# Kernel tuning notes

Hardware: AMD Instinct MI355X
Metric: run time of the kernel (lower is better)

## Reference

```python
import jax, jax.numpy as jnp
import numpy as np

NEG_SLOPE = 0.2


def gat_conv(x, src, dst, W, att_src, att_dst, bias, heads, out_ch, concat, N):
    # Linear transform: [N, heads, out_ch]
    h = (x @ W).reshape(N, heads, out_ch)
    # Per-node attention logits [N, heads]
    a_s = jnp.einsum('nhc,hc->nh', h, att_src)
    a_d = jnp.einsum('nhc,hc->nh', h, att_dst)
    # Per-edge logits: edge j->i uses src j, dst i
    e = jax.nn.leaky_relu(a_s[src] + a_d[dst], NEG_SLOPE)  # [E, heads]
    # Segment softmax over destination neighborhoods
    m = jax.ops.segment_max(e, dst, num_segments=N)  # [N, heads]
    ex = jnp.exp(e - m[dst])
    denom = jax.ops.segment_sum(ex, dst, num_segments=N)
    alpha = ex / denom[dst]  # [E, heads]
    # Weighted message scatter-add
    out = jax.ops.segment_sum(h[src] * alpha[:, :, None], dst, num_segments=N)  # [N, heads, out_ch]
    out = out.reshape(N, heads * out_ch) if concat else out.mean(axis=1)
    return out + bias


def setup_inputs() -> dict:
    key = jax.random.key(0)
    ks = jax.random.split(key, 12)
    N, E, F_IN, HID, HEADS, NCLS = 100000, 1600000, 256, 16, 8, 32
    x = jax.random.normal(ks[0], (N, F_IN), dtype=jnp.float32)
    edge_index = jax.random.randint(ks[1], (2, E), 0, N, dtype=jnp.int32)
    edge_weight = jax.random.uniform(ks[2], (E,), dtype=jnp.float32)
    s1 = 1.0 / np.sqrt(F_IN)
    W1 = jax.random.normal(ks[3], (F_IN, HEADS * HID), dtype=jnp.float32) * s1
    att_src1 = jax.random.normal(ks[4], (HEADS, HID), dtype=jnp.float32) * 0.1
    att_dst1 = jax.random.normal(ks[5], (HEADS, HID), dtype=jnp.float32) * 0.1
    b1 = jnp.zeros((HEADS * HID,), dtype=jnp.float32)
    s2 = 1.0 / np.sqrt(HEADS * HID)
    W2 = jax.random.normal(ks[6], (HEADS * HID, NCLS), dtype=jnp.float32) * s2
    att_src2 = jax.random.normal(ks[7], (1, NCLS), dtype=jnp.float32) * 0.1
    att_dst2 = jax.random.normal(ks[8], (1, NCLS), dtype=jnp.float32) * 0.1
    b2 = jnp.zeros((NCLS,), dtype=jnp.float32)
    return {"x": x, "edge_index": edge_index, "edge_weight": edge_weight,
            "W1": W1, "att_src1": att_src1, "att_dst1": att_dst1, "b1": b1,
            "W2": W2, "att_src2": att_src2, "att_dst2": att_dst2, "b2": b2}


def reference(x, edge_index, edge_weight, W1, att_src1, att_dst1, b1, W2, att_src2, att_dst2, b2):
    N = x.shape[0]
    # PyG GATConv add_self_loops=True: append self-loops once (used by both layers)
    loop = jnp.arange(N, dtype=edge_index.dtype)
    src = jnp.concatenate([edge_index[0], loop])
    dst = jnp.concatenate([edge_index[1], loop])
    # eval mode: dropout is identity; edge_weight unused by GATConv
    h = gat_conv(x, src, dst, W1, att_src1, att_dst1, b1, heads=8, out_ch=16, concat=True, N=N)
    h = jax.nn.elu(h)
    out = gat_conv(h, src, dst, W2, att_src2, att_dst2, b2, heads=1, out_ch=32, concat=False, N=N)
    return jax.nn.log_softmax(out, axis=-1)
```

## Files before the change

kernel.cpp:

```cpp
#include <hip/hip_runtime.h>
#include <hip/hip_fp16.h>
#include <math.h>

#define NEG_SLOPE 0.2f
#define NBLK 256

typedef _Float16 half8 __attribute__((ext_vector_type(8)));
typedef _Float16 half4 __attribute__((ext_vector_type(4)));
typedef float f32x4 __attribute__((ext_vector_type(4)));
typedef float f32x2 __attribute__((ext_vector_type(2)));

__device__ __forceinline__ float lrelu(float x){ return x > 0.f ? x : NEG_SLOPE*x; }

__global__ void k_prepw(const float* __restrict__ W, _Float16* __restrict__ Wt){
  int t = blockIdx.x*blockDim.x + threadIdx.x;
  int c = t >> 8, k = t & 255;
  Wt[t] = (_Float16)W[k*128 + c];
}

__global__ __launch_bounds__(256) void k_gemm1(const float* __restrict__ x,
                                               const _Float16* __restrict__ Wt,
                                               _Float16* __restrict__ h1h, int N){
  __shared__ _Float16 aL[2][128*40];
  __shared__ _Float16 bL[2][128*40];
  int tid = threadIdx.x;
  int w = tid >> 6, lane = tid & 63;
  int fq = lane >> 4, fr = lane & 15;
  int row0 = blockIdx.x * 128;
  f32x4 acc[2][8];
  #pragma unroll
  for (int m=0;m<2;m++)
    #pragma unroll
    for (int n=0;n<8;n++) acc[m][n] = (f32x4){0.f,0.f,0.f,0.f};

  int rA = tid>>3, kcA = (tid&7)*4;
  float4 va[4]; half8 vb[2];

  #pragma unroll
  for (int it=0; it<4; it++){
    int gr = row0 + it*32 + rA;
    va[it] = make_float4(0.f,0.f,0.f,0.f);
    if (gr < N) va[it] = *(const float4*)&x[(size_t)gr*256 + kcA];
  }
  #pragma unroll
  for (int it=0; it<2; it++){
    int chunk = it*256 + tid;
    vb[it] = *(const half8*)&Wt[(size_t)(chunk>>2)*256 + (chunk&3)*8];
  }
  #pragma unroll
  for (int it=0; it<4; it++){
    half4 hv; hv[0]=(_Float16)va[it].x; hv[1]=(_Float16)va[it].y;
    hv[2]=(_Float16)va[it].z; hv[3]=(_Float16)va[it].w;
    *(half4*)&aL[0][(it*32+rA)*40 + kcA] = hv;
  }
  #pragma unroll
  for (int it=0; it<2; it++){
    int chunk = it*256 + tid;
    *(half8*)&bL[0][(chunk>>2)*40 + (chunk&3)*8] = vb[it];
  }
  __syncthreads();

  int cur = 0;
  for (int ki=0; ki<8; ki++){
    int kk = ki*32;
    if (ki < 7){
      #pragma unroll
      for (int it=0; it<4; it++){
        int gr = row0 + it*32 + rA;
        va[it] = make_float4(0.f,0.f,0.f,0.f);
        if (gr < N) va[it] = *(const float4*)&x[(size_t)gr*256 + kk + 32 + kcA];
      }
      #pragma unroll
      for (int it=0; it<2; it++){
        int chunk = it*256 + tid;
        vb[it] = *(const half8*)&Wt[(size_t)(chunk>>2)*256 + kk + 32 + (chunk&3)*8];
      }
    }
    int kb = fq*8;
    half8 afrag[2], bfrag[8];
    #pragma unroll
    for (int m=0;m<2;m++) afrag[m] = *(half8*)&aL[cur][(w*32 + m*16 + fr)*40 + kb];
    #pragma unroll
    for (int n=0;n<8;n++) bfrag[n] = *(half8*)&bL[cur][(n*16 + fr)*40 + kb];
    #pragma unroll
    for (int m=0;m<2;m++)
      #pragma unroll
      for (int n=0;n<8;n++)
        acc[m][n] = __builtin_amdgcn_mfma_f32_16x16x32_f16(afrag[m], bfrag[n], acc[m][n], 0, 0, 0);
    if (ki < 7){
      #pragma unroll
      for (int it=0; it<4; it++){
        half4 hv; hv[0]=(_Float16)va[it].x; hv[1]=(_Float16)va[it].y;
        hv[2]=(_Float16)va[it].z; hv[3]=(_Float16)va[it].w;
        *(half4*)&aL[cur^1][(it*32+rA)*40 + kcA] = hv;
      }
      #pragma unroll
      for (int it=0; it<2; it++){
        int chunk = it*256 + tid;
        *(half8*)&bL[cur^1][(chunk>>2)*40 + (chunk&3)*8] = vb[it];
      }
      __syncthreads();
      cur ^= 1;
    }
  }
  #pragma unroll
  for (int m=0;m<2;m++){
    #pragma unroll
    for (int j=0;j<4;j++){
      int gr = row0 + w*32 + m*16 + fq*4 + j;
      if (gr < N){
        #pragma unroll
        for (int n=0;n<8;n++)
          h1h[(size_t)gr*128 + n*16 + fr] = (_Float16)acc[m][n][j];
      }
    }
  }
}

__global__ void k_cvt8(const _Float16* __restrict__ h1h,
                       const float* __restrict__ as_w, const float* __restrict__ ad_w,
                       unsigned* __restrict__ h1p, float* __restrict__ a_s,
                       float* __restrict__ a_d, int N){
  int t = blockIdx.x*blockDim.x + threadIdx.x;
  if (t >= N*16) return;
  int row = t >> 4, c8 = t & 15;
  half8 hv = *(const half8*)&h1h[(size_t)row*128 + c8*8];
  float f[8];
  #pragma unroll
  for (int j=0;j<8;j++) f[j] = (float)hv[j];
  int w0 = 0, w1 = 0;
  w0 = __builtin_amdgcn_cvt_pk_fp8_f32(f[0], f[1], w0, false);
  w0 = __builtin_amdgcn_cvt_pk_fp8_f32(f[2], f[3], w0, true);
  w1 = __builtin_amdgcn_cvt_pk_fp8_f32(f[4], f[5], w1, false);
  w1 = __builtin_amdgcn_cvt_pk_fp8_f32(f[6], f[7], w1, true);
  *(uint2*)&h1p[(size_t)row*32 + c8*2] = make_uint2((unsigned)w0,(unsigned)w1);
  int head = c8 >> 1;
  const float* wsp = &as_w[head*16 + (c8&1)*8];
  const float* wdp = &ad_w[head*16 + (c8&1)*8];
  float s=0.f, d=0.f;
  #pragma unroll
  for (int j=0;j<8;j++){ s = fmaf(f[j], wsp[j], s); d = fmaf(f[j], wdp[j], d); }
  s += __shfl_xor(s, 1);
  d += __shfl_xor(d, 1);
  if ((c8&1)==0){ a_s[(size_t)row*8+head]=s; a_d[(size_t)row*8+head]=d; }
}

__global__ __launch_bounds__(256) void k_bh(const int* __restrict__ dst, int* __restrict__ bh,
                                            int E, int EE, int NB){
  __shared__ int h[1024];
  int tid = threadIdx.x, blk = blockIdx.x;
  for (int i=tid;i<1024;i+=256) h[i]=0;
  __syncthreads();
  int chunk = (EE + NBLK - 1)/NBLK;
  int e0 = blk*chunk, e1 = min(e0+chunk, EE);
  for (int e=e0+tid; e<e1; e+=256){
    int d = (e<E)? dst[e] : (e-E);
    atomicAdd(&h[d>>7], 1);
  }
  __syncthreads();
  for (int i=tid;i<NB;i+=256) bh[i*NBLK + blk] = h[i];
}

__global__ __launch_bounds__(256) void k_scanA(int* __restrict__ bh, int* __restrict__ btot){
  __shared__ int t[256];
  int b = blockIdx.x, tid = threadIdx.x;
  int v = bh[b*NBLK + tid];
  t[tid] = v;
  __syncthreads();
  for (int off=1; off<256; off<<=1){
    int p = (tid>=off)? t[tid-off] : 0;
    __syncthreads();
    t[tid] += p;
    __syncthreads();
  }
  bh[b*NBLK + tid] = t[tid] - v;
  if (tid==255) btot[b] = t[255];
}

__global__ __launch_bounds__(256) void k_bscan(const int* __restrict__ btot, int* __restrict__ bbase,
                                               int* __restrict__ start_, int NB, int N, int EE){
  __shared__ int t[256];
  int tid = threadIdx.x;
  int i0 = tid*4;
  int a0 = (i0+0<NB)? btot[i0+0] : 0;
  int a1 = (i0+1<NB)? btot[i0+1] : 0;
  int a2 = (i0+2<NB)? btot[i0+2] : 0;
  int a3 = (i0+3<NB)? btot[i0+3] : 0;
  int s = a0+a1+a2+a3;
  t[tid] = s;
  __syncthreads();
  for (int off=1; off<256; off<<=1){
    int p = (tid>=off)? t[tid-off] : 0;
    __syncthreads();
    t[tid] += p;
    __syncthreads();
  }
  int excl = t[tid] - s;
  int e0=excl, e1=e0+a0, e2=e1+a1, e3=e2+a2;
  if (i0+0<NB) bbase[i0+0]=e0;
  if (i0+1<NB) bbase[i0+1]=e1;
  if (i0+2<NB) bbase[i0+2]=e2;
  if (i0+3<NB) bbase[i0+3]=e3;
  if (tid==0){ bbase[NB] = EE; start_[N] = EE; }
}

__global__ __launch_bounds__(256) void k_bfill(const int* __restrict__ src, const int* __restrict__ dst,
                       const int* __restrict__ bh, const int* __restrict__ bbase,
                       unsigned* __restrict__ pairs, int E, int EE, int NB){
  __shared__ int cur[1024];
  int tid = threadIdx.x, blk = blockIdx.x;
  for (int i=tid;i<NB;i+=256) cur[i] = bbase[i] + bh[i*NBLK + blk];
  __syncthreads();
  int chunk = (EE + NBLK - 1)/NBLK;
  int e0 = blk*chunk, e1 = min(e0+chunk, EE);
  for (int e=e0+tid; e<e1; e+=256){
    int s,d;
    if (e<E){ s=src[e]; d=dst[e]; } else { s=e-E; d=s; }
    int p = atomicAdd(&cur[d>>7], 1);
    pairs[p] = ((unsigned)s << 7) | (unsigned)(d & 127);
  }
}

__global__ __launch_bounds__(256) void k_pb(const int* __restrict__ bbase, const unsigned* __restrict__ pairs,
                    int* __restrict__ start_, int* __restrict__ csr_src, int N){
  __shared__ int hist[128];
  __shared__ int excl[128];
  int b = blockIdx.x;
  int tid = threadIdx.x;
  int base = bbase[b], cnt = bbase[b+1] - base;
  if (tid<128) hist[tid]=0;
  __syncthreads();
  for (int i=tid;i<cnt;i+=256){
    unsigned p = pairs[base+i];
    atomicAdd(&hist[p & 127], 1);
  }
  __syncthreads();
  if (tid < 128) excl[tid] = hist[tid];
  __syncthreads();
  for (int off=1; off<128; off<<=1){
    int p=0;
    if (tid<128 && tid>=off) p = excl[tid-off];
    __syncthreads();
    if (tid<128) excl[tid] += p;
    __syncthreads();
  }
  if (tid < 128){
    int e = excl[tid] - hist[tid];
    int node = (b<<7) + tid;
    if (node < N) start_[node] = base + e;
    hist[tid] = e;
  }
  __syncthreads();
  for (int i=tid;i<cnt;i+=256){
    unsigned p = pairs[base+i];
    int pos = atomicAdd(&hist[p & 127], 1);
    csr_src[base + pos] = (int)(p >> 7);
  }
}

__global__ __launch_bounds__(256) void k_agg1(const int* __restrict__ start, const int* __restrict__ csr_src,
                      const float* __restrict__ a_s, const float* __restrict__ a_d,
                      const unsigned* __restrict__ h1p, _Float16* __restrict__ acc1h, int N){
  int wid = (blockIdx.x*blockDim.x + threadIdx.x) >> 6;
  int lane = threadIdx.x & 63;
  if (wid >= N) return;
  int d = wid;
  int half = lane >> 5;
  int l32  = lane & 31;
  int head = l32 >> 2;
  float ad = a_d[(size_t)d*8 + head];
  int beg = start[d], end = start[d+1];
  float ax=0.f, ay=0.f, az=0.f, aw=0.f, den=0.f;
  int j = beg + half;
  for (; j + 6 < end; j += 8){
    int s0 = csr_src[j];
    int s1 = csr_src[j+2];
    int s2 = csr_src[j+4];
    int s3 = csr_src[j+6];
    float e0 = __expf(lrelu(a_s[(size_t)s0*8 + head] + ad));
    float e1 = __expf(lrelu(a_s[(size_t)s1*8 + head] + ad));
    float e2 = __expf(lrelu(a_s[(size_t)s2*8 + head] + ad));
    float e3 = __expf(lrelu(a_s[(size_t)s3*8 + head] + ad));
    unsigned u0 = h1p[(size_t)s0*32 + l32];
    unsigned u1 = h1p[(size_t)s1*32 + l32];
    unsigned u2 = h1p[(size_t)s2*32 + l32];
    unsigned u3 = h1p[(size_t)s3*32 + l32];
    f32x2 l0 = __builtin_amdgcn_cvt_pk_f32_fp8((int)u0, false), h0 = __builtin_amdgcn_cvt_pk_f32_fp8((int)u0, true);
    f32x2 l1 = __builtin_amdgcn_cvt_pk_f32_fp8((int)u1, false), h1 = __builtin_amdgcn_cvt_pk_f32_fp8((int)u1, true);
    f32x2 l2 = __builtin_amdgcn_cvt_pk_f32_fp8((int)u2, false), h2 = __builtin_amdgcn_cvt_pk_f32_fp8((int)u2, true);
    f32x2 l3 = __builtin_amdgcn_cvt_pk_f32_fp8((int)u3, false), h3 = __builtin_amdgcn_cvt_pk_f32_fp8((int)u3, true);
    ax = fmaf(e0, l0.x, ax); ay = fmaf(e0, l0.y, ay); az = fmaf(e0, h0.x, az); aw = fmaf(e0, h0.y, aw);
    ax = fmaf(e1, l1.x, ax); ay = fmaf(e1, l1.y, ay); az = fmaf(e1, h1.x, az); aw = fmaf(e1, h1.y, aw);
    ax = fmaf(e2, l2.x, ax); ay = fmaf(e2, l2.y, ay); az = fmaf(e2, h2.x, az); aw = fmaf(e2, h2.y, aw);
    ax = fmaf(e3, l3.x, ax); ay = fmaf(e3, l3.y, ay); az = fmaf(e3, h3.x, az); aw = fmaf(e3, h3.y, aw);
    den += (e0 + e1) + (e2 + e3);
  }
  for (; j < end; j += 2){
    int s0 = csr_src[j];
    float e0 = __expf(lrelu(a_s[(size_t)s0*8 + head] + ad));
    unsigned u0 = h1p[(size_t)s0*32 + l32];
    f32x2 l0 = __builtin_amdgcn_cvt_pk_f32_fp8((int)u0, false), h0 = __builtin_amdgcn_cvt_pk_f32_fp8((int)u0, true);
    ax = fmaf(e0, l0.x, ax); ay = fmaf(e0, l0.y, ay); az = fmaf(e0, h0.x, az); aw = fmaf(e0, h0.y, aw);
    den += e0;
  }
  ax += __shfl_xor(ax, 32);
  ay += __shfl_xor(ay, 32);
  az += __shfl_xor(az, 32);
  aw += __shfl_xor(aw, 32);
  den += __shfl_xor(den, 32);
  float inv = (den > 0.f) ? 1.f/den : 0.f;
  if (half == 0){
    half4 o;
    o[0]=(_Float16)(ax*inv); o[1]=(_Float16)(ay*inv);
    o[2]=(_Float16)(az*inv); o[3]=(_Float16)(aw*inv);
    *(half4*)&acc1h[(size_t)d*128 + l32*4] = o;
  }
}

__global__ __launch_bounds__(256) void k_layer2(const _Float16* __restrict__ acc1h, const float* __restrict__ b1,
                        const float* __restrict__ W2, const float* __restrict__ as2w,
                        const float* __restrict__ ad2w,
                        __half* __restrict__ h2ph, float* __restrict__ a_s2,
                        float* __restrict__ a_d2, int N){
  __shared__ float w2s[128][32];
  __shared__ float hs[8][128];
  int tid = threadIdx.x;
  #pragma unroll
  for (int it=0; it<16; it++){
    int idx = it*256 + tid;
    ((float*)w2s)[idx] = W2[idx];
  }
  int sub = tid>>5, ln = tid&31;
  int n = blockIdx.x*8 + sub;
  if (n < N){
    half4 hv = *(const half4*)&acc1h[(size_t)n*128 + ln*4];
    float4 bb = *(const float4*)&b1[ln*4];
    float v0 = (float)hv[0] + bb.x;
    float v1 = (float)hv[1] + bb.y;
    float v2 = (float)hv[2] + bb.z;
    float v3 = (float)hv[3] + bb.w;
    hs[sub][ln*4+0] = v0 > 0.f ? v0 : (__expf(v0) - 1.f);
    hs[sub][ln*4+1] = v1 > 0.f ? v1 : (__expf(v1) - 1.f);
    hs[sub][ln*4+2] = v2 > 0.f ? v2 : (__expf(v2) - 1.f);
    hs[sub][ln*4+3] = v3 > 0.f ? v3 : (__expf(v3) - 1.f);
  }
  __syncthreads();
  if (n >= N) return;
  float o = 0.f;
  #pragma unroll
  for (int k=0;k<128;k++) o = fmaf(hs[sub][k], w2s[k][ln], o);
  h2ph[(size_t)n*32+ln] = __float2half_rn(o);
  float ps = o*as2w[ln], pd = o*ad2w[ln];
  #pragma unroll
  for (int m=16;m;m>>=1){ ps += __shfl_xor(ps,m); pd += __shfl_xor(pd,m); }
  if (ln==0){ a_s2[n]=ps; a_d2[n]=pd; }
}

__global__ __launch_bounds__(256) void k_agg2(const int* __restrict__ start, const int* __restrict__ csr_src,
                      const float* __restrict__ a_s2, const float* __restrict__ a_d2,
                      const __half* __restrict__ h2ph, const float* __restrict__ b2,
                      float* __restrict__ out, int N){
  int g = (blockIdx.x*blockDim.x + threadIdx.x) >> 5;
  int ln = threadIdx.x & 31;
  if (g >= N) return;
  int d = g;
  int grp = ln >> 4;
  int l16 = ln & 15;
  float ad = a_d2[d];
  int beg = start[d], end = start[d+1];
  float accx=0.f, accy=0.f, den=0.f;
  int j = beg + grp;
  for (; j + 6 < end; j += 8){
    int s0 = csr_src[j];
    int s1 = csr_src[j+2];
    int s2 = csr_src[j+4];
    int s3 = csr_src[j+6];
    float e0 = __expf(lrelu(a_s2[s0] + ad));
    float e1 = __expf(lrelu(a_s2[s1] + ad));
    float e2 = __expf(lrelu(a_s2[s2] + ad));
    float e3 = __expf(lrelu(a_s2[s3] + ad));
    float2 v0 = __half22float2(*(const __half2*)&h2ph[(size_t)s0*32 + l16*2]);
    float2 v1 = __half22float2(*(const __half2*)&h2ph[(size_t)s1*32 + l16*2]);
    float2 v2 = __half22float2(*(const __half2*)&h2ph[(size_t)s2*32 + l16*2]);
    float2 v3 = __half22float2(*(const __half2*)&h2ph[(size_t)s3*32 + l16*2]);
    accx = fmaf(e0, v0.x, accx); accy = fmaf(e0, v0.y, accy);
    accx = fmaf(e1, v1.x, accx); accy = fmaf(e1, v1.y, accy);
    accx = fmaf(e2, v2.x, accx); accy = fmaf(e2, v2.y, accy);
    accx = fmaf(e3, v3.x, accx); accy = fmaf(e3, v3.y, accy);
    den += (e0 + e1) + (e2 + e3);
  }
  for (; j < end; j += 2){
    int s0 = csr_src[j];
    float e0 = __expf(lrelu(a_s2[s0] + ad));
    float2 v0 = __half22float2(*(const __half2*)&h2ph[(size_t)s0*32 + l16*2]);
    accx = fmaf(e0, v0.x, accx); accy = fmaf(e0, v0.y, accy);
    den += e0;
  }
  accx += __shfl_xor(accx, 16);
  accy += __shfl_xor(accy, 16);
  den  += __shfl_xor(den, 16);
  float2 bb = *(const float2*)&b2[l16*2];
  float vx = accx/den + bb.x;
  float vy = accy/den + bb.y;
  float mx = fmaxf(vx, vy);
  #pragma unroll
  for (int m=8;m;m>>=1) mx = fmaxf(mx, __shfl_xor(mx, m));
  float sm = __expf(vx-mx) + __expf(vy-mx);
  #pragma unroll
  for (int m=8;m;m>>=1) sm += __shfl_xor(sm, m);
  float lg = mx + __logf(sm);
  if (grp == 0){
    float2 o = make_float2(vx - lg, vy - lg);
    *(float2*)&out[(size_t)d*32 + l16*2] = o;
  }
}

extern "C" void kernel_launch(void* const* d_in, const int* in_sizes, int n_in,
                              void* d_out, int out_size, void* d_ws, size_t ws_size,
                              hipStream_t stream){
  const float* x   = (const float*)d_in[0];
  const int*   ei  = (const int*)d_in[1];
  const float* W1  = (const float*)d_in[3];
  const float* as1 = (const float*)d_in[4];
  const float* ad1 = (const float*)d_in[5];
  const float* b1  = (const float*)d_in[6];
  const float* W2  = (const float*)d_in[7];
  const float* as2 = (const float*)d_in[8];
  const float* ad2 = (const float*)d_in[9];
  const float* b2  = (const float*)d_in[10];

  int N  = in_sizes[0] / 256;
  int E  = in_sizes[2];
  int EE = E + N;
  const int* src = ei;
  const int* dst = ei + E;

  int NB = (N + 127) >> 7;

  int* iw = (int*)d_ws;
  int* bh      = iw;                 iw += 1024*NBLK;
  int* btot    = iw;                 iw += 1024;
  int* bbase   = iw;                 iw += 1028;
  int* start_  = iw;                 iw += ((N+1+3)/4)*4;
  int* csr_src = iw;                 iw += ((EE+3)/4)*4;

  float* w = (float*)iw;
  float* a_s1   = w; w += (size_t)N*8;
  float* a_d1   = w; w += (size_t)N*8;
  float* a_s2   = w; w += (size_t)N;
  float* a_d2   = w; w += (size_t)N;
  _Float16* acc1h = (_Float16*)w; w += (size_t)N*64;
  _Float16* h1h  = (_Float16*)w; w += (size_t)N*64;
  _Float16* h2ph = (_Float16*)w; w += (size_t)N*16;
  _Float16* Wt   = (_Float16*)w; w += 32768/2;
  unsigned* h1p  = (unsigned*)w; w += (size_t)N*16;
  float* out    = (float*)d_out;

  unsigned* pairs = (unsigned*)acc1h;

  hipLaunchKernelGGL(k_prepw, dim3(128), dim3(256), 0, stream, W1, Wt);
  hipLaunchKernelGGL(k_gemm1, dim3((N+127)/128), dim3(256), 0, stream, x, Wt, h1h, N);
  hipLaunchKernelGGL(k_cvt8, dim3((N*16+255)/256), dim3(256), 0, stream, h1h, as1, ad1, h1p, a_s1, a_d1, N);
  hipLaunchKernelGGL(k_bh,    dim3(NBLK), dim3(256), 0, stream, dst, bh, E, EE, NB);
  hipLaunchKernelGGL(k_scanA, dim3(NB),   dim3(256), 0, stream, bh, btot);
  hipLaunchKernelGGL(k_bscan, dim3(1),    dim3(256), 0, stream, btot, bbase, start_, NB, N, EE);
  hipLaunchKernelGGL(k_bfill, dim3(NBLK), dim3(256), 0, stream, src, dst, bh, bbase, pairs, E, EE, NB);
  hipLaunchKernelGGL(k_pb,    dim3(NB),   dim3(256), 0, stream, bbase, pairs, start_, csr_src, N);
  hipLaunchKernelGGL(k_agg1, dim3((N+3)/4), dim3(256), 0, stream, start_, csr_src, a_s1, a_d1, h1p, acc1h, N);
  hipLaunchKernelGGL(k_layer2, dim3((N+7)/8), dim3(256), 0, stream, acc1h, b1, W2, as2, ad2, (__half*)h2ph, a_s2, a_d2, N);
  hipLaunchKernelGGL(k_agg2, dim3((N+7)/8), dim3(256), 0, stream, start_, csr_src, a_s2, a_d2, (const __half*)h2ph, b2, out, N);
}
```

Baseline: 259.8 us.

## Fuse FP8 packing and attention logits into GEMM1 epilogue via permuted W columns

Permutes the transposed W1 columns so each MFMA lane holds eight contiguous output channels. The GEMM epilogue can then pack them to FP8 and compute the per-head attention logits directly, which removes the separate conversion kernel and the fp16 intermediate round-trip through memory. The layer-1 aggregation is reorganized so 16 lanes each handle 8 channels across 4 edge groups, using 8-byte gathers. In exchange it adds register pressure to the GEMM epilogue and needs an extra shuffle-reduction stage in aggregation.

```diff
diff --git a/kernel.cpp b/kernel.cpp
--- a/kernel.cpp
+++ b/kernel.cpp
@@ -14,13 +14,18 @@
 
 __global__ void k_prepw(const float* __restrict__ W, _Float16* __restrict__ Wt){
   int t = blockIdx.x*blockDim.x + threadIdx.x;
-  int c = t >> 8, k = t & 255;
+  int p = t >> 8, k = t & 255;
+  int c = ((p & 15) << 3) | (p >> 4);
   Wt[t] = (_Float16)W[k*128 + c];
 }
 
 __global__ __launch_bounds__(256) void k_gemm1(const float* __restrict__ x,
                                                const _Float16* __restrict__ Wt,
-                                               _Float16* __restrict__ h1h, int N){
+                                               const float* __restrict__ as_w,
+                                               const float* __restrict__ ad_w,
+                                               unsigned* __restrict__ h1p,
+                                               float* __restrict__ a_s,
+                                               float* __restrict__ a_d, int N){
   __shared__ _Float16 aL[2][128*40];
   __shared__ _Float16 bL[2][128*40];
   int tid = threadIdx.x;
@@ -103,46 +108,33 @@
       cur ^= 1;
     }
   }
+  int head = fr >> 1;
+  const float* wsp = &as_w[head*16 + (fr&1)*8];
+  const float* wdp = &ad_w[head*16 + (fr&1)*8];
   #pragma unroll
   for (int m=0;m<2;m++){
     #pragma unroll
     for (int j=0;j<4;j++){
       int gr = row0 + w*32 + m*16 + fq*4 + j;
       if (gr < N){
+        float f[8];
         #pragma unroll
-        for (int n=0;n<8;n++)
-          h1h[(size_t)gr*128 + n*16 + fr] = (_Float16)acc[m][n][j];
+        for (int n=0;n<8;n++) f[n] = acc[m][n][j];
+        int w0 = 0, w1 = 0;
+        w0 = __builtin_amdgcn_cvt_pk_fp8_f32(f[0], f[1], w0, false);
+        w0 = __builtin_amdgcn_cvt_pk_fp8_f32(f[2], f[3], w0, true);
+        w1 = __builtin_amdgcn_cvt_pk_fp8_f32(f[4], f[5], w1, false);
+        w1 = __builtin_amdgcn_cvt_pk_fp8_f32(f[6], f[7], w1, true);
+        *(uint2*)&h1p[(size_t)gr*32 + fr*2] = make_uint2((unsigned)w0,(unsigned)w1);
+        float s=0.f, dd=0.f;
+        #pragma unroll
+        for (int n=0;n<8;n++){ s = fmaf(f[n], wsp[n], s); dd = fmaf(f[n], wdp[n], dd); }
+        s  += __shfl_xor(s, 1);
+        dd += __shfl_xor(dd, 1);
+        if (!(fr & 1)){ a_s[(size_t)gr*8+head] = s; a_d[(size_t)gr*8+head] = dd; }
       }
     }
   }
-}
-
-__global__ void k_cvt8(const _Float16* __restrict__ h1h,
-                       const float* __restrict__ as_w, const float* __restrict__ ad_w,
-                       unsigned* __restrict__ h1p, float* __restrict__ a_s,
-                       float* __restrict__ a_d, int N){
-  int t = blockIdx.x*blockDim.x + threadIdx.x;
-  if (t >= N*16) return;
-  int row = t >> 4, c8 = t & 15;
-  half8 hv = *(const half8*)&h1h[(size_t)row*128 + c8*8];
-  float f[8];
-  #pragma unroll
-  for (int j=0;j<8;j++) f[j] = (float)hv[j];
-  int w0 = 0, w1 = 0;
-  w0 = __builtin_amdgcn_cvt_pk_fp8_f32(f[0], f[1], w0, false);
-  w0 = __builtin_amdgcn_cvt_pk_fp8_f32(f[2], f[3], w0, true);
-  w1 = __builtin_amdgcn_cvt_pk_fp8_f32(f[4], f[5], w1, false);
-  w1 = __builtin_amdgcn_cvt_pk_fp8_f32(f[6], f[7], w1, true);
-  *(uint2*)&h1p[(size_t)row*32 + c8*2] = make_uint2((unsigned)w0,(unsigned)w1);
-  int head = c8 >> 1;
-  const float* wsp = &as_w[head*16 + (c8&1)*8];
-  const float* wdp = &ad_w[head*16 + (c8&1)*8];
-  float s=0.f, d=0.f;
-  #pragma unroll
-  for (int j=0;j<8;j++){ s = fmaf(f[j], wsp[j], s); d = fmaf(f[j], wdp[j], d); }
-  s += __shfl_xor(s, 1);
-  d += __shfl_xor(d, 1);
-  if ((c8&1)==0){ a_s[(size_t)row*8+head]=s; a_d[(size_t)row*8+head]=d; }
 }
 
 __global__ __launch_bounds__(256) void k_bh(const int* __restrict__ dst, int* __restrict__ bh,
@@ -265,55 +257,52 @@
   int lane = threadIdx.x & 63;
   if (wid >= N) return;
   int d = wid;
-  int half = lane >> 5;
-  int l32  = lane & 31;
-  int head = l32 >> 2;
+  int grp = lane >> 4;
+  int fr  = lane & 15;
+  int head = fr >> 1;
   float ad = a_d[(size_t)d*8 + head];
   int beg = start[d], end = start[d+1];
-  float ax=0.f, ay=0.f, az=0.f, aw=0.f, den=0.f;
-  int j = beg + half;
-  for (; j + 6 < end; j += 8){
+  float a0=0.f,a1=0.f,a2=0.f,a3=0.f,a4=0.f,a5=0.f,a6=0.f,a7=0.f,den=0.f;
+  int j = beg + grp;
+  for (; j + 4 < end; j += 8){
     int s0 = csr_src[j];
-    int s1 = csr_src[j+2];
-    int s2 = csr_src[j+4];
-    int s3 = csr_src[j+6];
+    int s1 = csr_src[j+4];
     float e0 = __expf(lrelu(a_s[(size_t)s0*8 + head] + ad));
     float e1 = __expf(lrelu(a_s[(size_t)s1*8 + head] + ad));
-    float e2 = __expf(lrelu(a_s[(size_t)s2*8 + head] + ad));
-    float e3 = __expf(lrelu(a_s[(size_t)s3*8 + head] + ad));
-    unsigned u0 = h1p[(size_t)s0*32 + l32];
-    unsigned u1 = h1p[(size_t)s1*32 + l32];
-    unsigned u2 = h1p[(size_t)s2*32 + l32];
-    unsigned u3 = h1p[(size_t)s3*32 + l32];
-    f32x2 l0 = __builtin_amdgcn_cvt_pk_f32_fp8((int)u0, false), h0 = __builtin_amdgcn_cvt_pk_f32_fp8((int)u0, true);
-    f32x2 l1 = __builtin_amdgcn_cvt_pk_f32_fp8((int)u1, false), h1 = __builtin_amdgcn_cvt_pk_f32_fp8((int)u1, true);
-    f32x2 l2 = __builtin_amdgcn_cvt_pk_f32_fp8((int)u2, false), h2 = __builtin_amdgcn_cvt_pk_f32_fp8((int)u2, true);
-    f32x2 l3 = __builtin_amdgcn_cvt_pk_f32_fp8((int)u3, false), h3 = __builtin_amdgcn_cvt_pk_f32_fp8((int)u3, true);
-    ax = fmaf(e0, l0.x, ax); ay = fmaf(e0, l0.y, ay); az = fmaf(e0, h0.x, az); aw = fmaf(e0, h0.y, aw);
-    ax = fmaf(e1, l1.x, ax); ay = fmaf(e1, l1.y, ay); az = fmaf(e1, h1.x, az); aw = fmaf(e1, h1.y, aw);
-    ax = fmaf(e2, l2.x, ax); ay = fmaf(e2, l2.y, ay); az = fmaf(e2, h2.x, az); aw = fmaf(e2, h2.y, aw);
-    ax = fmaf(e3, l3.x, ax); ay = fmaf(e3, l3.y, ay); az = fmaf(e3, h3.x, az); aw = fmaf(e3, h3.y, aw);
-    den += (e0 + e1) + (e2 + e3);
-  }
-  for (; j < end; j += 2){
+    uint2 u0 = *(const uint2*)&h1p[(size_t)s0*32 + fr*2];
+    uint2 u1 = *(const uint2*)&h1p[(size_t)s1*32 + fr*2];
+    f32x2 p0 = __builtin_amdgcn_cvt_pk_f32_fp8((int)u0.x, false), p1 = __builtin_amdgcn_cvt_pk_f32_fp8((int)u0.x, true);
+    f32x2 p2 = __builtin_amdgcn_cvt_pk_f32_fp8((int)u0.y, false), p3 = __builtin_amdgcn_cvt_pk_f32_fp8((int)u0.y, true);
+    f32x2 q0 = __builtin_amdgcn_cvt_pk_f32_fp8((int)u1.x, false), q1 = __builtin_amdgcn_cvt_pk_f32_fp8((int)u1.x, true);
+    f32x2 q2 = __builtin_amdgcn_cvt_pk_f32_fp8((int)u1.y, false), q3 = __builtin_amdgcn_cvt_pk_f32_fp8((int)u1.y, true);
+    a0 = fmaf(e0, p0.x, a0); a1 = fmaf(e0, p0.y, a1); a2 = fmaf(e0, p1.x, a2); a3 = fmaf(e0, p1.y, a3);
+    a4 = fmaf(e0, p2.x, a4); a5 = fmaf(e0, p2.y, a5); a6 = fmaf(e0, p3.x, a6); a7 = fmaf(e0, p3.y, a7);
+    a0 = fmaf(e1, q0.x, a0); a1 = fmaf(e1, q0.y, a1); a2 = fmaf(e1, q1.x, a2); a3 = fmaf(e1, q1.y, a3);
+    a4 = fmaf(e1, q2.x, a4); a5 = fmaf(e1, q2.y, a5); a6 = fmaf(e1, q3.x, a6); a7 = fmaf(e1, q3.y, a7);
+    den += e0 + e1;
+  }
+  if (j < end){
     int s0 = csr_src[j];
     float e0 = __expf(lrelu(a_s[(size_t)s0*8 + head] + ad));
-    unsigned u0 = h1p[(size_t)s0*32 + l32];
-    f32x2 l0 = __builtin_amdgcn_cvt_pk_f32_fp8((int)u0, false), h0 = __builtin_amdgcn_cvt_pk_f32_fp8((int)u0, true);
-    ax = fmaf(e0, l0.x, ax); ay = fmaf(e0, l0.y, ay); az = fmaf(e0, h0.x, az); aw = fmaf(e0, h0.y, aw);
+    uint2 u0 = *(const uint2*)&h1p[(size_t)s0*32 + fr*2];
+    f32x2 p0 = __builtin_amdgcn_cvt_pk_f32_fp8((int)u0.x, false), p1 = __builtin_amdgcn_cvt_pk_f32_fp8((int)u0.x, true);
+    f32x2 p2 = __builtin_amdgcn_cvt_pk_f32_fp8((int)u0.y, false), p3 = __builtin_amdgcn_cvt_pk_f32_fp8((int)u0.y, true);
+    a0 = fmaf(e0, p0.x, a0); a1 = fmaf(e0, p0.y, a1); a2 = fmaf(e0, p1.x, a2); a3 = fmaf(e0, p1.y, a3);
+    a4 = fmaf(e0, p2.x, a4); a5 = fmaf(e0, p2.y, a5); a6 = fmaf(e0, p3.x, a6); a7 = fmaf(e0, p3.y, a7);
     den += e0;
   }
-  ax += __shfl_xor(ax, 32);
-  ay += __shfl_xor(ay, 32);
-  az += __shfl_xor(az, 32);
-  aw += __shfl_xor(aw, 32);
-  den += __shfl_xor(den, 32);
+  a0 += __shfl_xor(a0,16); a1 += __shfl_xor(a1,16); a2 += __shfl_xor(a2,16); a3 += __shfl_xor(a3,16);
+  a4 += __shfl_xor(a4,16); a5 += __shfl_xor(a5,16); a6 += __shfl_xor(a6,16); a7 += __shfl_xor(a7,16);
+  den += __shfl_xor(den,16);
+  a0 += __shfl_xor(a0,32); a1 += __shfl_xor(a1,32); a2 += __shfl_xor(a2,32); a3 += __shfl_xor(a3,32);
+  a4 += __shfl_xor(a4,32); a5 += __shfl_xor(a5,32); a6 += __shfl_xor(a6,32); a7 += __shfl_xor(a7,32);
+  den += __shfl_xor(den,32);
   float inv = (den > 0.f) ? 1.f/den : 0.f;
-  if (half == 0){
-    half4 o;
-    o[0]=(_Float16)(ax*inv); o[1]=(_Float16)(ay*inv);
-    o[2]=(_Float16)(az*inv); o[3]=(_Float16)(aw*inv);
-    *(half4*)&acc1h[(size_t)d*128 + l32*4] = o;
+  if (grp == 0){
+    half8 o;
+    o[0]=(_Float16)(a0*inv); o[1]=(_Float16)(a1*inv); o[2]=(_Float16)(a2*inv); o[3]=(_Float16)(a3*inv);
+    o[4]=(_Float16)(a4*inv); o[5]=(_Float16)(a5*inv); o[6]=(_Float16)(a6*inv); o[7]=(_Float16)(a7*inv);
+    *(half8*)&acc1h[(size_t)d*128 + fr*8] = o;
   }
 }
 
@@ -450,7 +439,6 @@
   float* a_s2   = w; w += (size_t)N;
   float* a_d2   = w; w += (size_t)N;
   _Float16* acc1h = (_Float16*)w; w += (size_t)N*64;
-  _Float16* h1h  = (_Float16*)w; w += (size_t)N*64;
   _Float16* h2ph = (_Float16*)w; w += (size_t)N*16;
   _Float16* Wt   = (_Float16*)w; w += 32768/2;
   unsigned* h1p  = (unsigned*)w; w += (size_t)N*16;
@@ -459,8 +447,7 @@
   unsigned* pairs = (unsigned*)acc1h;
 
   hipLaunchKernelGGL(k_prepw, dim3(128), dim3(256), 0, stream, W1, Wt);
-  hipLaunchKernelGGL(k_gemm1, dim3((N+127)/128), dim3(256), 0, stream, x, Wt, h1h, N);
-  hipLaunchKernelGGL(k_cvt8, dim3((N*16+255)/256), dim3(256), 0, stream, h1h, as1, ad1, h1p, a_s1, a_d1, N);
+  hipLaunchKernelGGL(k_gemm1, dim3((N+127)/128), dim3(256), 0, stream, x, Wt, as1, ad1, h1p, a_s1, a_d1, N);
   hipLaunchKernelGGL(k_bh,    dim3(NBLK), dim3(256), 0, stream, dst, bh, E, EE, NB);
   hipLaunchKernelGGL(k_scanA, dim3(NB),   dim3(256), 0, stream, bh, btot);
   hipLaunchKernelGGL(k_bscan, dim3(1),    dim3(256), 0, stream, btot, bbase, start_, NB, N, EE);
```

New measurement: 251.2 us. 1.03x faster.
